# Performance work log

Measured on AMD Instinct MI355X. Metric: run time of the kernel, lower is better.

The kernel has to match this reference:

```python
import jax, jax.numpy as jnp
import numpy as np

EPS = 1e-12
SAMPLE_SIZES = (100, 50)  # hardcoded in the torch module


def setup_inputs() -> dict:
    key = jax.random.key(0)
    k1, k2, k3, k4 = jax.random.split(key, 4)
    N, E, C_IN, C_HID, C_OUT = 50000, 1600000, 256, 64, 128
    x = jax.random.normal(k1, (N, C_IN), dtype=jnp.float32)
    edge_index = jax.random.randint(k2, (2, E), 0, N, dtype=jnp.int64)
    W1 = jax.random.normal(k3, (C_IN, C_HID), dtype=jnp.float32) / np.sqrt(C_IN)
    b1 = jnp.zeros((C_HID,), dtype=jnp.float32)
    W2 = jax.random.normal(k4, (C_HID, C_OUT), dtype=jnp.float32) / np.sqrt(C_HID)
    b2 = jnp.zeros((C_OUT,), dtype=jnp.float32)
    return {"x": x, "edge_index": edge_index, "W1": W1, "b1": b1, "W2": W2, "b2": b2}


def _sample_mask(edge_index, num_samples, key):
    """Keep at most num_samples random out-edges per source node (fixed-shape mask)."""
    src = edge_index[0]
    E = src.shape[0]
    pri = jax.random.uniform(key, (E,))
    order = jnp.lexsort((pri, src))            # group by src, random order within group
    src_sorted = src[order]
    first = jnp.searchsorted(src_sorted, src_sorted, side="left")
    rank = jnp.arange(E) - first               # rank within each src group
    keep_sorted = rank < num_samples
    mask = jnp.zeros((E,), dtype=jnp.float32).at[order].set(keep_sorted.astype(jnp.float32))
    return mask


def _gcn_conv(x, edge_index, edge_weight, W, b, num_nodes):
    """PyG GCNConv: self-loops + symmetric deg^-1/2 normalization, aggregate at dst."""
    h = x @ W                                   # [N, out]
    src, dst = edge_index[0], edge_index[1]
    loop = jnp.arange(num_nodes, dtype=src.dtype)
    src_f = jnp.concatenate([src, loop])
    dst_f = jnp.concatenate([dst, loop])
    w_f = jnp.concatenate([edge_weight, jnp.ones((num_nodes,), dtype=edge_weight.dtype)])
    deg = jax.ops.segment_sum(w_f, dst_f, num_segments=num_nodes)
    dinv = jnp.where(deg > 0, jax.lax.rsqrt(jnp.maximum(deg, EPS)), 0.0)
    norm = w_f * dinv[src_f] * dinv[dst_f]      # [E+N]
    msgs = h[src_f] * norm[:, None]             # gather + scale (memory bound)
    out = jax.ops.segment_sum(msgs, dst_f, num_segments=num_nodes)
    return out + b


def reference(x, edge_index, W1, b1, W2, b2):
    num_nodes = x.shape[0]
    skey = jax.random.key(42)
    sk1, sk2 = jax.random.split(skey)
    m1 = _sample_mask(edge_index, SAMPLE_SIZES[0], sk1)
    m2 = _sample_mask(edge_index, SAMPLE_SIZES[1], sk2)
    h = _gcn_conv(x, edge_index, m1, W1, b1, num_nodes)
    h = jax.nn.relu(h)
    h = h / jnp.maximum(jnp.linalg.norm(h, axis=-1, keepdims=True), EPS)  # F.normalize(p=2)
    out = _gcn_conv(h, edge_index, m2, W2, b2, num_nodes)
    return out
```

## Files before the change

### kernel.cpp

```cpp
#include <hip/hip_runtime.h>

typedef unsigned int u32;
typedef unsigned short u16;
typedef unsigned long long u64;
typedef __attribute__((ext_vector_type(8))) short bh8;
typedef __attribute__((ext_vector_type(4))) float f4;

#define HMAX 1024
#define MAXD 128
#define SB_CAP 24576
#define DB_CAP 6144
#define SBCHUNK 2048
#define SPLIT 8
#define G1S 136
#define DROP_CAP 32768

__device__ inline f4 mfma16(bh8 a, bh8 b, f4 c) {
  return __builtin_amdgcn_mfma_f32_16x16x32_bf16(a, b, c, 0, 0, 0);
}

__host__ __device__ inline void tf2x32(u32 k0, u32 k1, u32 x0, u32 x1, u32& o0, u32& o1) {
  u32 ks2 = k0 ^ k1 ^ 0x1BD11BDAu;
#define ROTL32(x,d) (((x)<<(d))|((x)>>(32-(d))))
#define TFR(r) { x0 += x1; x1 = ROTL32(x1,(r)); x1 ^= x0; }
  x0 += k0; x1 += k1;
  TFR(13) TFR(15) TFR(26) TFR(6)
  x0 += k1; x1 += ks2 + 1u;
  TFR(17) TFR(29) TFR(16) TFR(24)
  x0 += ks2; x1 += k0 + 2u;
  TFR(13) TFR(15) TFR(26) TFR(6)
  x0 += k0; x1 += k1 + 3u;
  TFR(17) TFR(29) TFR(16) TFR(24)
  x0 += k1; x1 += ks2 + 4u;
  TFR(13) TFR(15) TFR(26) TFR(6)
  x0 += ks2; x1 += k0 + 5u;
  o0 = x0; o1 = x1;
#undef TFR
#undef ROTL32
}

__device__ inline u16 f2bf(float f) {
  u32 u = __float_as_uint(f);
  return (u16)((u + 0x7FFFu + ((u >> 16) & 1u)) >> 16);
}
__device__ inline float bflo(u32 u) { return __uint_as_float(u << 16); }
__device__ inline float bfhi(u32 u) { return __uint_as_float(u & 0xFFFF0000u); }

struct BinS { u32 lsrc[128]; u32 lbase[128]; u32 ldst[512]; u32 dbase[512]; };
struct GemS { u16 xs[64 * G1S]; u16 ws[64 * G1S]; };

__global__ __launch_bounds__(256) void k_mega1(const int* __restrict__ ei, int E,
                                               const float* __restrict__ x, int N,
                                               const float* __restrict__ W1, const float* __restrict__ W2,
                                               int* __restrict__ srcCnt, u32* __restrict__ srcRec,
                                               int* __restrict__ dstCnt, u64* __restrict__ dstRec,
                                               u16* __restrict__ h1b, u16* __restrict__ W2t, int nBin) {
  __shared__ __align__(16) char smem[sizeof(GemS)];
  int t = threadIdx.x;
  int bid = blockIdx.x;

  if (bid < nBin) {
    BinS& S = *(BinS*)smem;
    if (t < 128) S.lsrc[t] = 0;
    for (int v = t; v < 512; v += 256) S.ldst[v] = 0;
    __syncthreads();
    int lo = bid * SBCHUNK;
    int hi = min(lo + SBCHUNK, E);
    int e0 = lo + 8 * t;
    int nv = min(8, hi - e0); if (nv < 0) nv = 0;
    int sv[8], dv[8];
    if (nv == 8 && ((E & 3) == 0)) {
      int4 a0 = *((const int4*)(ei + e0));
      int4 a1 = *((const int4*)(ei + e0 + 4));
      int4 b0 = *((const int4*)(ei + E + e0));
      int4 b1 = *((const int4*)(ei + E + e0 + 4));
      sv[0]=a0.x; sv[1]=a0.y; sv[2]=a0.z; sv[3]=a0.w; sv[4]=a1.x; sv[5]=a1.y; sv[6]=a1.z; sv[7]=a1.w;
      dv[0]=b0.x; dv[1]=b0.y; dv[2]=b0.z; dv[3]=b0.w; dv[4]=b1.x; dv[5]=b1.y; dv[6]=b1.z; dv[7]=b1.w;
    } else {
      for (int j = 0; j < nv; ++j) { sv[j] = ei[e0 + j]; dv[j] = ei[E + e0 + j]; }
    }
    for (int j = 0; j < nv; ++j) {
      atomicAdd(&S.lsrc[sv[j] >> 9], 1u);
      atomicAdd(&S.ldst[dv[j] >> 7], 1u);
    }
    __syncthreads();
    if (t < 128) {
      u32 c = S.lsrc[t];
      if (c) S.lbase[t] = (u32)atomicAdd(&srcCnt[t], (int)c);
      S.lsrc[t] = 0;
    }
    for (int v = t; v < 512; v += 256) {
      u32 cd = S.ldst[v];
      if (cd) S.dbase[v] = (u32)atomicAdd(&dstCnt[v], (int)cd);
      S.ldst[v] = 0;
    }
    __syncthreads();
    for (int j = 0; j < nv; ++j) {
      int s = sv[j], d = dv[j];
      u32 i = (u32)(e0 + j);
      int bs = s >> 9;
      u32 slot = S.lbase[bs] + atomicAdd(&S.lsrc[bs], 1u);
      if (slot < SB_CAP) srcRec[(size_t)bs * SB_CAP + slot] = ((u32)(s & 511) << 21) | i;
      int bd = d >> 7;
      u32 slot2 = S.dbase[bd] + atomicAdd(&S.ldst[bd], 1u);
      if (slot2 < DB_CAP)
        dstRec[(size_t)bd * DB_CAP + slot2] = ((u64)(d & 127) << 37) | ((u64)(u32)s << 21) | i;
    }
  } else if (bid < 2 * nBin) {
    GemS& G = *(GemS*)smem;
    int wv = t >> 6, lane = t & 63;
    int qd = lane >> 4, md = lane & 15;
    int m0 = (bid - nBin) * 64;
    if (m0 >= N) return;
    f4 acc[4] = {};
    for (int ks = 0; ks < 256; ks += 128) {
      __syncthreads();
#pragma unroll
      for (int i = 0; i < 8; ++i) {
        int f = t + 256 * i;
        int r = f >> 5, c4 = f & 31;
        int grow = m0 + r; if (grow >= N) grow = N - 1;
        float4 v = ((const float4*)x)[(size_t)grow * 64 + (ks >> 2) + c4];
        u32 p0 = (u32)f2bf(v.x) | ((u32)f2bf(v.y) << 16);
        u32 p1 = (u32)f2bf(v.z) | ((u32)f2bf(v.w) << 16);
        *((uint2*)(G.xs + r * G1S + c4 * 4)) = make_uint2(p0, p1);
      }
#pragma unroll
      for (int i = 0; i < 8; ++i) {
        int f = t + 256 * i;
        int k = f >> 4, c4 = f & 15;
        float4 v = ((const float4*)W1)[(ks + k) * 16 + c4];
        int n0 = c4 * 4;
        G.ws[(n0 + 0) * G1S + k] = f2bf(v.x);
        G.ws[(n0 + 1) * G1S + k] = f2bf(v.y);
        G.ws[(n0 + 2) * G1S + k] = f2bf(v.z);
        G.ws[(n0 + 3) * G1S + k] = f2bf(v.w);
      }
      __syncthreads();
#pragma unroll
      for (int kk = 0; kk < 128; kk += 32) {
        bh8 af = *((const bh8*)(G.xs + (16 * wv + md) * G1S + kk + qd * 8));
#pragma unroll
        for (int nt = 0; nt < 4; ++nt) {
          bh8 bf = *((const bh8*)(G.ws + (nt * 16 + md) * G1S + kk + qd * 8));
          acc[nt] = mfma16(af, bf, acc[nt]);
        }
      }
    }
#pragma unroll
    for (int nt = 0; nt < 4; ++nt)
#pragma unroll
      for (int r = 0; r < 4; ++r) {
        int row = m0 + 16 * wv + qd * 4 + r;
        if (row < N) h1b[(size_t)row * 64 + nt * 16 + md] = f2bf(acc[nt][r]);
      }
  } else {
    for (int e = t; e < 64 * 128; e += 256) {
      int n = e & 127, k = e >> 7;
      W2t[n * 64 + k] = f2bf(W2[k * 128 + n]);
    }
  }
}

__global__ __launch_bounds__(256) void k_shist(const int* __restrict__ srcCnt, const u32* __restrict__ srcRec,
                                               int* __restrict__ outdegB) {
  int bk = blockIdx.x >> 3;
  int part = blockIdx.x & (SPLIT - 1);
  int total = min(srcCnt[bk], SB_CAP);
  int lo = total * part / SPLIT;
  int hi = total * (part + 1) / SPLIT;
  __shared__ u32 cnt[512];
  int t = threadIdx.x;
  cnt[t] = 0; cnt[t + 256] = 0;
  __syncthreads();
  const u32* R = srcRec + (size_t)bk * SB_CAP;
  for (int i = lo + t; i < hi; i += 256) atomicAdd(&cnt[R[i] >> 21], 1u);
  __syncthreads();
  int base = bk * 512;
  for (int v = t; v < 512; v += 256) {
    u32 c = cnt[v];
    if (c) atomicAdd(&outdegB[base + v], (int)c);
  }
}

__global__ __launch_bounds__(256) void k_hdetect(const int* __restrict__ outdegB, u32* __restrict__ idAB,
                                                 int* __restrict__ hcA, int* __restrict__ hcB,
                                                 const int* __restrict__ dstCnt, int* __restrict__ bucketBase,
                                                 int* __restrict__ dptr, int nbD, int N) {
  if (blockIdx.x == 0 && threadIdx.x == 0) {
    int s = 0;
    for (int i = 0; i < nbD; ++i) { bucketBase[i] = s; s += min(dstCnt[i], DB_CAP); }
    bucketBase[nbD] = s;
    dptr[N] = s;
  }
  int v = blockIdx.x * 256 + threadIdx.x;
  if (v >= N) return;
  int dg = outdegB[v];
  u32 pk = 0;
  if (dg > 50) {
    int idb = atomicAdd(hcB, 1);
    if (idb < HMAX) pk = (u32)(idb + 1);
    if (dg > 100) {
      int ida = atomicAdd(hcA, 1);
      if (ida < HMAX) pk |= (u32)(ida + 1) << 16;
    }
  }
  idAB[v] = pk;
}

__global__ __launch_bounds__(256) void k_hfill(const int* __restrict__ srcCnt, const u32* __restrict__ srcRec,
                                               const u32* __restrict__ idAB,
                                               int* __restrict__ bcA, u64* __restrict__ bukA,
                                               int* __restrict__ bcB, u64* __restrict__ bukB,
                                               u32 kaA, u32 kbA, u32 kaB, u32 kbB) {
  int bk = blockIdx.x >> 3;
  int part = blockIdx.x & (SPLIT - 1);
  int total = min(srcCnt[bk], SB_CAP);
  int lo = total * part / SPLIT;
  int hi = total * (part + 1) / SPLIT;
  const u32* R = srcRec + (size_t)bk * SB_CAP;
  int base = bk * 512;
  for (int i = lo + threadIdx.x; i < hi; i += 256) {
    u32 r = R[i];
    u32 pk = idAB[base + (int)(r >> 21)];
    if (pk) {
      u32 e = r & 0x1FFFFFu;
      int idb = (int)(pk & 0xFFFFu) - 1;
      if (idb >= 0) {
        u32 w0, w1; tf2x32(kaB, kbB, 0u, e, w0, w1);
        int slot = atomicAdd(&bcB[idb], 1);
        if (slot < MAXD) bukB[(size_t)idb * MAXD + slot] = ((u64)((w0 ^ w1) >> 9) << 32) | e;
      }
      int ida = (int)(pk >> 16) - 1;
      if (ida >= 0) {
        u32 w0, w1; tf2x32(kaA, kbA, 0u, e, w0, w1);
        int slot = atomicAdd(&bcA[ida], 1);
        if (slot < MAXD) bukA[(size_t)ida * MAXD + slot] = ((u64)((w0 ^ w1) >> 9) << 32) | e;
      }
    }
  }
}

__global__ __launch_bounds__(256) void k_rank2(const int* __restrict__ hcA, const int* __restrict__ bcA,
                                               const u64* __restrict__ bukA,
                                               const int* __restrict__ hcB, const int* __restrict__ bcB,
                                               const u64* __restrict__ bukB,
                                               int* __restrict__ dropCnt, u32* __restrict__ dropList) {
  bool isA = blockIdx.x < (HMAX / 4);
  int bx = isA ? blockIdx.x : blockIdx.x - HMAX / 4;
  const int* hcount = isA ? hcA : hcB;
  const int* bcount = isA ? bcA : bcB;
  const u64* bucket = isA ? bukA : bukB;
  int S = isA ? 100 : 50;
  u32 bit = isA ? 1u : 2u;
  int wid = (bx * 256 + (int)threadIdx.x) >> 6;
  int lane = threadIdx.x & 63;
  int hc = hcount[0]; if (hc > HMAX) hc = HMAX;
  if (wid >= hc) return;
  int d = bcount[wid]; if (d > MAXD) d = MAXD;
  const u64* B = bucket + (size_t)wid * MAXD;
  for (int i = lane; i < d; i += 64) {
    u64 ki = B[i];
    int rank = 0;
    for (int j = 0; j < d; ++j) rank += (B[j] < ki) ? 1 : 0;
    if (rank >= S) {
      int idx = atomicAdd(dropCnt, 1);
      if (idx < DROP_CAP) dropList[idx] = ((u32)ki & 0x1FFFFFu) | (bit << 21);
    }
  }
}

__global__ __launch_bounds__(256) void k_phase2(const int* __restrict__ bucketBase,
                                                const int* __restrict__ dstCnt,
                                                const u64* __restrict__ dstRec,
                                                const int* __restrict__ dropCnt,
                                                const u32* __restrict__ dropList,
                                                u32* __restrict__ entries, int* __restrict__ dptr,
                                                float* __restrict__ dinv1, float* __restrict__ dinv2, int N) {
  int b = blockIdx.x;
  int base = bucketBase[b];
  int cnt0 = min(dstCnt[b], DB_CAP);
  const u64* R = dstRec + (size_t)b * DB_CAP;
  __shared__ u32 cnt[128];
  __shared__ u32 htab[4096];
  __shared__ u32 ws2[2];
  int t = threadIdx.x;
  if (t < 128) cnt[t] = 0;
  for (int i = t; i < 4096; i += 256) htab[i] = 0xFFFFFFFFu;
  __syncthreads();
  int dc = min(dropCnt[0], 3072);
  for (int i = t; i < dc; i += 256) {
    u32 pk = dropList[i];
    u32 key = pk & 0x1FFFFFu;
    u32 h = (key * 2654435761u) >> 20;
    while (true) {
      u32 old = atomicCAS(&htab[h], 0xFFFFFFFFu, pk);
      if (old == 0xFFFFFFFFu) break;
      if ((old & 0x1FFFFFu) == key) { atomicOr(&htab[h], pk & 0x00600000u); break; }
      h = (h + 1) & 4095;
    }
  }
  __syncthreads();
  for (int i = t; i < cnt0; i += 256) {
    u64 r = R[i];
    u32 dl = (u32)(r >> 37) & 127u;
    u32 key = (u32)r & 0x1FFFFFu;
    u32 drop = 0;
    u32 h = (key * 2654435761u) >> 20;
    while (true) {
      u32 v = htab[h];
      if (v == 0xFFFFFFFFu) break;
      if ((v & 0x1FFFFFu) == key) { drop = (v >> 21) & 3u; break; }
      h = (h + 1) & 4095;
    }
    u32 add = 1u + ((1u - (drop & 1u)) << 10) + ((1u - ((drop >> 1) & 1u)) << 20);
    atomicAdd(&cnt[dl], add);
  }
  __syncthreads();
  u32 c0 = (t < 128) ? cnt[t] : 0;
  u32 tot = c0 & 1023u;
  int lane = t & 63, w = t >> 6;
  u32 incl = tot;
  for (int off = 1; off < 64; off <<= 1) {
    u32 nbv = (u32)__shfl_up((int)incl, off, 64);
    if (lane >= off) incl += nbv;
  }
  if (lane == 63 && w == 0) ws2[0] = incl;
  __syncthreads();
  u32 excl = incl - tot + ((w == 1) ? ws2[0] : 0u);
  int v0 = b * 128 + t;
  if (t < 128 && v0 < N) {
    dptr[v0] = base + (int)excl;
    dinv1[v0] = 1.0f / sqrtf((float)(((c0 >> 10) & 1023u) + 1u));
    dinv2[v0] = 1.0f / sqrtf((float)(((c0 >> 20) & 1023u) + 1u));
  }
  __syncthreads();
  if (t < 128) cnt[t] = excl;
  __syncthreads();
  for (int i = t; i < cnt0; i += 256) {
    u64 r = R[i];
    u32 dl = (u32)(r >> 37) & 127u;
    u32 key = (u32)r & 0x1FFFFFu;
    u32 drop = 0;
    u32 h = (key * 2654435761u) >> 20;
    while (true) {
      u32 v = htab[h];
      if (v == 0xFFFFFFFFu) break;
      if ((v & 0x1FFFFFu) == key) { drop = (v >> 21) & 3u; break; }
      h = (h + 1) & 4095;
    }
    u32 src = (u32)(r >> 21) & 0xFFFFu;
    u32 slot = atomicAdd(&cnt[dl], 1u);
    entries[base + slot] = src | ((drop & 1u) ? 0u : (1u << 30)) | ((drop & 2u) ? 0u : (1u << 31));
  }
}

__global__ __launch_bounds__(256) void k_conv1n(const int* __restrict__ ptr, const u32* __restrict__ entries,
                                                const float* __restrict__ dinv1, const uint4* __restrict__ h1q,
                                                const float* __restrict__ b1, uint4* __restrict__ hnbq, int N) {
  int wid = (blockIdx.x * 256 + threadIdx.x) >> 6;
  if (wid >= N) return;
  int lane = threadIdx.x & 63;
  int lo8 = lane & 7, grp = lane >> 3;
  int beg = ptr[wid], end = ptr[wid + 1];
  float a0 = 0.f, a1 = 0.f, a2 = 0.f, a3 = 0.f, a4 = 0.f, a5 = 0.f, a6 = 0.f, a7 = 0.f;
  for (int cb = beg; cb < end; cb += 64) {
    int idx = cb + lane;
    float wgt = 0.f; int s = 0;
    if (idx < end) {
      u32 e = entries[idx];
      s = (int)(e & 0xFFFFu);
      if (e & (1u << 30)) wgt = dinv1[s];
    }
    int nq = (min(64, end - cb) + 7) >> 3;
    int j = grp;
    float w = __shfl(wgt, j, 64);
    int sj = __shfl(s, j, 64);
    uint4 uv = h1q[(size_t)sj * 8 + lo8];
    for (int i = 1; i < nq; ++i) {
      int j2 = j + 8;
      float w2 = __shfl(wgt, j2, 64);
      int s2 = __shfl(s, j2, 64);
      uint4 uv2 = h1q[(size_t)s2 * 8 + lo8];
      a0 = fmaf(w, bflo(uv.x), a0); a1 = fmaf(w, bfhi(uv.x), a1);
      a2 = fmaf(w, bflo(uv.y), a2); a3 = fmaf(w, bfhi(uv.y), a3);
      a4 = fmaf(w, bflo(uv.z), a4); a5 = fmaf(w, bfhi(uv.z), a5);
      a6 = fmaf(w, bflo(uv.w), a6); a7 = fmaf(w, bfhi(uv.w), a7);
      w = w2; uv = uv2; j = j2;
    }
    a0 = fmaf(w, bflo(uv.x), a0); a1 = fmaf(w, bfhi(uv.x), a1);
    a2 = fmaf(w, bflo(uv.y), a2); a3 = fmaf(w, bfhi(uv.y), a3);
    a4 = fmaf(w, bflo(uv.z), a4); a5 = fmaf(w, bfhi(uv.z), a5);
    a6 = fmaf(w, bflo(uv.w), a6); a7 = fmaf(w, bfhi(uv.w), a7);
  }
#pragma unroll
  for (int off = 8; off < 64; off <<= 1) {
    a0 += __shfl_xor(a0, off, 64); a1 += __shfl_xor(a1, off, 64);
    a2 += __shfl_xor(a2, off, 64); a3 += __shfl_xor(a3, off, 64);
    a4 += __shfl_xor(a4, off, 64); a5 += __shfl_xor(a5, off, 64);
    a6 += __shfl_xor(a6, off, 64); a7 += __shfl_xor(a7, off, 64);
  }
  float dv = dinv1[wid];
  uint4 uo = h1q[(size_t)wid * 8 + lo8];
  a0 = fmaf(dv, bflo(uo.x), a0); a1 = fmaf(dv, bfhi(uo.x), a1);
  a2 = fmaf(dv, bflo(uo.y), a2); a3 = fmaf(dv, bfhi(uo.y), a3);
  a4 = fmaf(dv, bflo(uo.z), a4); a5 = fmaf(dv, bfhi(uo.z), a5);
  a6 = fmaf(dv, bflo(uo.w), a6); a7 = fmaf(dv, bfhi(uo.w), a7);
  float4 bbA = ((const float4*)b1)[lo8 * 2];
  float4 bbB = ((const float4*)b1)[lo8 * 2 + 1];
  float o0 = fmaxf(fmaf(dv, a0, bbA.x), 0.f);
  float o1 = fmaxf(fmaf(dv, a1, bbA.y), 0.f);
  float o2 = fmaxf(fmaf(dv, a2, bbA.z), 0.f);
  float o3 = fmaxf(fmaf(dv, a3, bbA.w), 0.f);
  float o4 = fmaxf(fmaf(dv, a4, bbB.x), 0.f);
  float o5 = fmaxf(fmaf(dv, a5, bbB.y), 0.f);
  float o6 = fmaxf(fmaf(dv, a6, bbB.z), 0.f);
  float o7 = fmaxf(fmaf(dv, a7, bbB.w), 0.f);
  float ss = fmaf(o0, o0, fmaf(o1, o1, fmaf(o2, o2, o3 * o3)))
           + fmaf(o4, o4, fmaf(o5, o5, fmaf(o6, o6, o7 * o7)));
#pragma unroll
  for (int off = 1; off < 8; off <<= 1) ss += __shfl_xor(ss, off, 8);
  float sc = 1.f / fmaxf(sqrtf(ss), 1e-12f);
  if (lane < 8) {
    uint4 pv;
    pv.x = (u32)f2bf(o0 * sc) | ((u32)f2bf(o1 * sc) << 16);
    pv.y = (u32)f2bf(o2 * sc) | ((u32)f2bf(o3 * sc) << 16);
    pv.z = (u32)f2bf(o4 * sc) | ((u32)f2bf(o5 * sc) << 16);
    pv.w = (u32)f2bf(o6 * sc) | ((u32)f2bf(o7 * sc) << 16);
    hnbq[(size_t)wid * 8 + lo8] = pv;
  }
}

__global__ __launch_bounds__(256) void k_agg2(const int* __restrict__ ptr, const u32* __restrict__ entries,
                                              const float* __restrict__ dinv2, const uint4* __restrict__ hnq,
                                              uint4* __restrict__ agg2q, int N) {
  int wid = (blockIdx.x * 256 + threadIdx.x) >> 6;
  if (wid >= N) return;
  int lane = threadIdx.x & 63;
  int lo8 = lane & 7, grp = lane >> 3;
  int beg = ptr[wid], end = ptr[wid + 1];
  float a0 = 0.f, a1 = 0.f, a2 = 0.f, a3 = 0.f, a4 = 0.f, a5 = 0.f, a6 = 0.f, a7 = 0.f;
  for (int cb = beg; cb < end; cb += 64) {
    int idx = cb + lane;
    float wgt = 0.f; int s = 0;
    if (idx < end) {
      u32 e = entries[idx];
      s = (int)(e & 0xFFFFu);
      if (e & (1u << 31)) wgt = dinv2[s];
    }
    int nq = (min(64, end - cb) + 7) >> 3;
    int j = grp;
    float w = __shfl(wgt, j, 64);
    int sj = __shfl(s, j, 64);
    uint4 uv = hnq[(size_t)sj * 8 + lo8];
    for (int i = 1; i < nq; ++i) {
      int j2 = j + 8;
      float w2 = __shfl(wgt, j2, 64);
      int s2 = __shfl(s, j2, 64);
      uint4 uv2 = hnq[(size_t)s2 * 8 + lo8];
      a0 = fmaf(w, bflo(uv.x), a0); a1 = fmaf(w, bfhi(uv.x), a1);
      a2 = fmaf(w, bflo(uv.y), a2); a3 = fmaf(w, bfhi(uv.y), a3);
      a4 = fmaf(w, bflo(uv.z), a4); a5 = fmaf(w, bfhi(uv.z), a5);
      a6 = fmaf(w, bflo(uv.w), a6); a7 = fmaf(w, bfhi(uv.w), a7);
      w = w2; uv = uv2; j = j2;
    }
    a0 = fmaf(w, bflo(uv.x), a0); a1 = fmaf(w, bfhi(uv.x), a1);
    a2 = fmaf(w, bflo(uv.y), a2); a3 = fmaf(w, bfhi(uv.y), a3);
    a4 = fmaf(w, bflo(uv.z), a4); a5 = fmaf(w, bfhi(uv.z), a5);
    a6 = fmaf(w, bflo(uv.w), a6); a7 = fmaf(w, bfhi(uv.w), a7);
  }
#pragma unroll
  for (int off = 8; off < 64; off <<= 1) {
    a0 += __shfl_xor(a0, off, 64); a1 += __shfl_xor(a1, off, 64);
    a2 += __shfl_xor(a2, off, 64); a3 += __shfl_xor(a3, off, 64);
    a4 += __shfl_xor(a4, off, 64); a5 += __shfl_xor(a5, off, 64);
    a6 += __shfl_xor(a6, off, 64); a7 += __shfl_xor(a7, off, 64);
  }
  float dv = dinv2[wid];
  uint4 uo = hnq[(size_t)wid * 8 + lo8];
  a0 = fmaf(dv, bflo(uo.x), a0); a1 = fmaf(dv, bfhi(uo.x), a1);
  a2 = fmaf(dv, bflo(uo.y), a2); a3 = fmaf(dv, bfhi(uo.y), a3);
  a4 = fmaf(dv, bflo(uo.z), a4); a5 = fmaf(dv, bfhi(uo.z), a5);
  a6 = fmaf(dv, bflo(uo.w), a6); a7 = fmaf(dv, bfhi(uo.w), a7);
  if (lane < 8) {
    uint4 pv;
    pv.x = (u32)f2bf(dv * a0) | ((u32)f2bf(dv * a1) << 16);
    pv.y = (u32)f2bf(dv * a2) | ((u32)f2bf(dv * a3) << 16);
    pv.z = (u32)f2bf(dv * a4) | ((u32)f2bf(dv * a5) << 16);
    pv.w = (u32)f2bf(dv * a6) | ((u32)f2bf(dv * a7) << 16);
    agg2q[(size_t)wid * 8 + lo8] = pv;
  }
}

#define G2S 72
__global__ __launch_bounds__(256) void k_gemm2f(const u16* __restrict__ aggb, const u16* __restrict__ W2t,
                                                const float* __restrict__ b2, float* __restrict__ out, int N) {
  __shared__ u16 hs[64 * G2S];
  __shared__ u16 ws[128 * G2S];
  int t = threadIdx.x;
  int wv = t >> 6, lane = t & 63;
  int qd = lane >> 4, md = lane & 15;
  int m0 = blockIdx.x * 64;
#pragma unroll
  for (int i = 0; i < 2; ++i) {
    int cc = t + 256 * i;
    int r = cc >> 3, kc = (cc & 7) * 8;
    int grow = m0 + r; if (grow >= N) grow = N - 1;
    *((uint4*)(hs + r * G2S + kc)) = *((const uint4*)(aggb + (size_t)grow * 64 + kc));
  }
#pragma unroll
  for (int i = 0; i < 4; ++i) {
    int cc = t + 256 * i;
    int n = cc >> 3, kc = (cc & 7) * 8;
    *((uint4*)(ws + n * G2S + kc)) = *((const uint4*)(W2t + n * 64 + kc));
  }
  __syncthreads();
  f4 acc[8] = {};
#pragma unroll
  for (int kk = 0; kk < 64; kk += 32) {
    bh8 af = *((const bh8*)(hs + (16 * wv + md) * G2S + kk + qd * 8));
#pragma unroll
    for (int nt = 0; nt < 8; ++nt) {
      bh8 bf = *((const bh8*)(ws + (nt * 16 + md) * G2S + kk + qd * 8));
      acc[nt] = mfma16(af, bf, acc[nt]);
    }
  }
#pragma unroll
  for (int nt = 0; nt < 8; ++nt) {
    float bv = b2[nt * 16 + md];
#pragma unroll
    for (int r = 0; r < 4; ++r) {
      int row = m0 + 16 * wv + qd * 4 + r;
      if (row < N) out[(size_t)row * 128 + nt * 16 + md] = acc[nt][r] + bv;
    }
  }
}

extern "C" void kernel_launch(void* const* d_in, const int* in_sizes, int n_in,
                              void* d_out, int out_size, void* d_ws, size_t ws_size,
                              hipStream_t stream) {
  const float* x  = (const float*)d_in[0];
  const int*   ei = (const int*)d_in[1];
  const float* W1 = (const float*)d_in[2];
  const float* b1 = (const float*)d_in[3];
  const float* W2 = (const float*)d_in[4];
  const float* b2 = (const float*)d_in[5];
  const int N = in_sizes[0] / 256;
  const int E = in_sizes[1] / 2;
  const int nbS = (N + 511) >> 9;
  const int nbD = (N + 127) >> 7;

  u32 sk1a, sk1b, sk2a, sk2b;
  tf2x32(0u, 42u, 0u, 0u, sk1a, sk1b);
  tf2x32(0u, 42u, 0u, 1u, sk2a, sk2b);

  char* p = (char*)d_ws;
  auto alloc = [&](size_t bytes) { char* r = p; p += (bytes + 255) & ~(size_t)255; return r; };
  int* dstCnt      = (int*)alloc(512 * 4);
  int* srcCnt      = (int*)alloc(128 * 4);
  int* hcbA        = (int*)alloc((size_t)(1 + HMAX) * 4);
  int* hcbB        = (int*)alloc((size_t)(1 + HMAX) * 4);
  int* outdegB     = (int*)alloc((size_t)nbS * 512 * 4);
  int* dropCnt     = (int*)alloc(256);
  char* zero_end = p;
  u32* dropList = (u32*)alloc((size_t)DROP_CAP * 4);
  u32* idAB     = (u32*)alloc((size_t)nbS * 512 * 4);
  u16* h1b      = (u16*)alloc((size_t)N * 64 * 2);
  u16* hnb      = (u16*)alloc((size_t)N * 64 * 2);
  u16* agg2b    = (u16*)alloc((size_t)N * 64 * 2);
  float* dinv1  = (float*)alloc((size_t)N * 4);
  float* dinv2  = (float*)alloc((size_t)N * 4);
  int* dptr     = (int*)alloc((size_t)(N + 1) * 4);
  int* bucketBase = (int*)alloc(513 * 4);
  u32* entries  = (u32*)alloc((size_t)E * 4);
  u32* srcRec   = (u32*)alloc((size_t)nbS * SB_CAP * 4);
  u64* dstRec   = (u64*)alloc((size_t)nbD * DB_CAP * 8);
  u64* bukA     = (u64*)alloc((size_t)HMAX * MAXD * 8);
  u64* bukB     = (u64*)alloc((size_t)HMAX * MAXD * 8);
  u16* W2t      = (u16*)alloc(64 * 128 * 2);

  int* hcA = hcbA; int* bcA = hcbA + 1;
  int* hcB = hcbB; int* bcB = hcbB + 1;

  hipMemsetAsync(dstCnt, 0x00, (size_t)(zero_end - (char*)dstCnt), stream);

  const int nBin = (E + SBCHUNK - 1) / SBCHUNK;
  const int nGemm = (N + 63) / 64;
  k_mega1<<<nBin + nGemm + 1, 256, 0, stream>>>(ei, E, x, N, W1, W2,
                                                srcCnt, srcRec, dstCnt, dstRec, h1b, W2t, nBin);
  k_shist<<<nbS * SPLIT, 256, 0, stream>>>(srcCnt, srcRec, outdegB);
  k_hdetect<<<(N + 255) / 256, 256, 0, stream>>>(outdegB, idAB, hcA, hcB, dstCnt, bucketBase,
                                                 dptr, nbD, N);
  k_hfill<<<nbS * SPLIT, 256, 0, stream>>>(srcCnt, srcRec, idAB, bcA, bukA, bcB, bukB,
                                           sk1a, sk1b, sk2a, sk2b);
  k_rank2<<<HMAX / 2, 256, 0, stream>>>(hcA, bcA, bukA, hcB, bcB, bukB, dropCnt, dropList);
  k_phase2<<<nbD, 256, 0, stream>>>(bucketBase, dstCnt, dstRec, dropCnt, dropList,
                                    entries, dptr, dinv1, dinv2, N);
  k_conv1n<<<(N * 64 + 255) / 256, 256, 0, stream>>>(dptr, entries, dinv1, (const uint4*)h1b, b1,
                                                     (uint4*)hnb, N);
  k_agg2<<<(N * 64 + 255) / 256, 256, 0, stream>>>(dptr, entries, dinv2, (const uint4*)hnb,
                                                   (uint4*)agg2b, N);
  k_gemm2f<<<(N + 63) / 64, 256, 0, stream>>>(agg2b, W2t, b2, (float*)d_out, N);
}
```

Baseline: 303.8 us.

## Drop source-binning pass; count out-degree with global atomics and scan edges directly

Replaces the source-bucket record scatter and the separate histogram kernel with direct global atomic increments of per-node out-degree inside the binning kernel. The hub-fill kernel now streams the raw source array instead of the binned records. This removes a kernel launch plus the srcRec write and two reads of it, in exchange for 1.6M scattered global atomics and a grid-stride scan over all edges. The first GEMM also switches to a 64-wide K tile with smaller LDS (stride 72), which raises occupancy but adds more sync steps; it also fixes the GEMM block range to use nGemm.

```diff
diff --git a/kernel.cpp b/kernel.cpp
--- a/kernel.cpp
+++ b/kernel.cpp
@@ -8,11 +8,9 @@
 
 #define HMAX 1024
 #define MAXD 128
-#define SB_CAP 24576
 #define DB_CAP 6144
 #define SBCHUNK 2048
-#define SPLIT 8
-#define G1S 136
+#define G1S 72
 #define DROP_CAP 32768
 
 __device__ inline f4 mfma16(bh8 a, bh8 b, f4 c) {
@@ -46,22 +44,22 @@
 __device__ inline float bflo(u32 u) { return __uint_as_float(u << 16); }
 __device__ inline float bfhi(u32 u) { return __uint_as_float(u & 0xFFFF0000u); }
 
-struct BinS { u32 lsrc[128]; u32 lbase[128]; u32 ldst[512]; u32 dbase[512]; };
+struct BinS { u32 ldst[512]; u32 dbase[512]; };
 struct GemS { u16 xs[64 * G1S]; u16 ws[64 * G1S]; };
 
 __global__ __launch_bounds__(256) void k_mega1(const int* __restrict__ ei, int E,
                                                const float* __restrict__ x, int N,
                                                const float* __restrict__ W1, const float* __restrict__ W2,
-                                               int* __restrict__ srcCnt, u32* __restrict__ srcRec,
+                                               int* __restrict__ outdeg,
                                                int* __restrict__ dstCnt, u64* __restrict__ dstRec,
                                                u16* __restrict__ h1b, u16* __restrict__ W2t, int nBin) {
   __shared__ __align__(16) char smem[sizeof(GemS)];
   int t = threadIdx.x;
   int bid = blockIdx.x;
+  int nGemm = (N + 63) >> 6;
 
   if (bid < nBin) {
     BinS& S = *(BinS*)smem;
-    if (t < 128) S.lsrc[t] = 0;
     for (int v = t; v < 512; v += 256) S.ldst[v] = 0;
     __syncthreads();
     int lo = bid * SBCHUNK;
@@ -80,15 +78,10 @@
       for (int j = 0; j < nv; ++j) { sv[j] = ei[e0 + j]; dv[j] = ei[E + e0 + j]; }
     }
     for (int j = 0; j < nv; ++j) {
-      atomicAdd(&S.lsrc[sv[j] >> 9], 1u);
+      atomicAdd(&outdeg[sv[j]], 1);
       atomicAdd(&S.ldst[dv[j] >> 7], 1u);
     }
     __syncthreads();
-    if (t < 128) {
-      u32 c = S.lsrc[t];
-      if (c) S.lbase[t] = (u32)atomicAdd(&srcCnt[t], (int)c);
-      S.lsrc[t] = 0;
-    }
     for (int v = t; v < 512; v += 256) {
       u32 cd = S.ldst[v];
       if (cd) S.dbase[v] = (u32)atomicAdd(&dstCnt[v], (int)cd);
@@ -98,27 +91,24 @@
     for (int j = 0; j < nv; ++j) {
       int s = sv[j], d = dv[j];
       u32 i = (u32)(e0 + j);
-      int bs = s >> 9;
-      u32 slot = S.lbase[bs] + atomicAdd(&S.lsrc[bs], 1u);
-      if (slot < SB_CAP) srcRec[(size_t)bs * SB_CAP + slot] = ((u32)(s & 511) << 21) | i;
       int bd = d >> 7;
       u32 slot2 = S.dbase[bd] + atomicAdd(&S.ldst[bd], 1u);
       if (slot2 < DB_CAP)
         dstRec[(size_t)bd * DB_CAP + slot2] = ((u64)(d & 127) << 37) | ((u64)(u32)s << 21) | i;
     }
-  } else if (bid < 2 * nBin) {
+  } else if (bid < nBin + nGemm) {
     GemS& G = *(GemS*)smem;
     int wv = t >> 6, lane = t & 63;
     int qd = lane >> 4, md = lane & 15;
     int m0 = (bid - nBin) * 64;
     if (m0 >= N) return;
     f4 acc[4] = {};
-    for (int ks = 0; ks < 256; ks += 128) {
+    for (int ks = 0; ks < 256; ks += 64) {
       __syncthreads();
 #pragma unroll
-      for (int i = 0; i < 8; ++i) {
+      for (int i = 0; i < 4; ++i) {
         int f = t + 256 * i;
-        int r = f >> 5, c4 = f & 31;
+        int r = f >> 4, c4 = f & 15;
         int grow = m0 + r; if (grow >= N) grow = N - 1;
         float4 v = ((const float4*)x)[(size_t)grow * 64 + (ks >> 2) + c4];
         u32 p0 = (u32)f2bf(v.x) | ((u32)f2bf(v.y) << 16);
@@ -126,7 +116,7 @@
         *((uint2*)(G.xs + r * G1S + c4 * 4)) = make_uint2(p0, p1);
       }
 #pragma unroll
-      for (int i = 0; i < 8; ++i) {
+      for (int i = 0; i < 4; ++i) {
         int f = t + 256 * i;
         int k = f >> 4, c4 = f & 15;
         float4 v = ((const float4*)W1)[(ks + k) * 16 + c4];
@@ -138,7 +128,7 @@
       }
       __syncthreads();
 #pragma unroll
-      for (int kk = 0; kk < 128; kk += 32) {
+      for (int kk = 0; kk < 64; kk += 32) {
         bh8 af = *((const bh8*)(G.xs + (16 * wv + md) * G1S + kk + qd * 8));
 #pragma unroll
         for (int nt = 0; nt < 4; ++nt) {
@@ -162,28 +152,7 @@
   }
 }
 
-__global__ __launch_bounds__(256) void k_shist(const int* __restrict__ srcCnt, const u32* __restrict__ srcRec,
-                                               int* __restrict__ outdegB) {
-  int bk = blockIdx.x >> 3;
-  int part = blockIdx.x & (SPLIT - 1);
-  int total = min(srcCnt[bk], SB_CAP);
-  int lo = total * part / SPLIT;
-  int hi = total * (part + 1) / SPLIT;
-  __shared__ u32 cnt[512];
-  int t = threadIdx.x;
-  cnt[t] = 0; cnt[t + 256] = 0;
-  __syncthreads();
-  const u32* R = srcRec + (size_t)bk * SB_CAP;
-  for (int i = lo + t; i < hi; i += 256) atomicAdd(&cnt[R[i] >> 21], 1u);
-  __syncthreads();
-  int base = bk * 512;
-  for (int v = t; v < 512; v += 256) {
-    u32 c = cnt[v];
-    if (c) atomicAdd(&outdegB[base + v], (int)c);
-  }
-}
-
-__global__ __launch_bounds__(256) void k_hdetect(const int* __restrict__ outdegB, u32* __restrict__ idAB,
+__global__ __launch_bounds__(256) void k_hdetect(const int* __restrict__ outdeg, u32* __restrict__ idAB,
                                                  int* __restrict__ hcA, int* __restrict__ hcB,
                                                  const int* __restrict__ dstCnt, int* __restrict__ bucketBase,
                                                  int* __restrict__ dptr, int nbD, int N) {
@@ -195,7 +164,7 @@
   }
   int v = blockIdx.x * 256 + threadIdx.x;
   if (v >= N) return;
-  int dg = outdegB[v];
+  int dg = outdeg[v];
   u32 pk = 0;
   if (dg > 50) {
     int idb = atomicAdd(hcB, 1);
@@ -208,34 +177,27 @@
   idAB[v] = pk;
 }
 
-__global__ __launch_bounds__(256) void k_hfill(const int* __restrict__ srcCnt, const u32* __restrict__ srcRec,
+__global__ __launch_bounds__(256) void k_hfill(const int* __restrict__ ei, int E,
                                                const u32* __restrict__ idAB,
                                                int* __restrict__ bcA, u64* __restrict__ bukA,
                                                int* __restrict__ bcB, u64* __restrict__ bukB,
                                                u32 kaA, u32 kbA, u32 kaB, u32 kbB) {
-  int bk = blockIdx.x >> 3;
-  int part = blockIdx.x & (SPLIT - 1);
-  int total = min(srcCnt[bk], SB_CAP);
-  int lo = total * part / SPLIT;
-  int hi = total * (part + 1) / SPLIT;
-  const u32* R = srcRec + (size_t)bk * SB_CAP;
-  int base = bk * 512;
-  for (int i = lo + threadIdx.x; i < hi; i += 256) {
-    u32 r = R[i];
-    u32 pk = idAB[base + (int)(r >> 21)];
+  for (int e = blockIdx.x * 256 + (int)threadIdx.x; e < E; e += (int)gridDim.x * 256) {
+    int s = ei[e];
+    u32 pk = idAB[s];
     if (pk) {
-      u32 e = r & 0x1FFFFFu;
+      u32 eu = (u32)e;
       int idb = (int)(pk & 0xFFFFu) - 1;
       if (idb >= 0) {
-        u32 w0, w1; tf2x32(kaB, kbB, 0u, e, w0, w1);
+        u32 w0, w1; tf2x32(kaB, kbB, 0u, eu, w0, w1);
         int slot = atomicAdd(&bcB[idb], 1);
-        if (slot < MAXD) bukB[(size_t)idb * MAXD + slot] = ((u64)((w0 ^ w1) >> 9) << 32) | e;
+        if (slot < MAXD) bukB[(size_t)idb * MAXD + slot] = ((u64)((w0 ^ w1) >> 9) << 32) | eu;
       }
       int ida = (int)(pk >> 16) - 1;
       if (ida >= 0) {
-        u32 w0, w1; tf2x32(kaA, kbA, 0u, e, w0, w1);
+        u32 w0, w1; tf2x32(kaA, kbA, 0u, eu, w0, w1);
         int slot = atomicAdd(&bcA[ida], 1);
-        if (slot < MAXD) bukA[(size_t)ida * MAXD + slot] = ((u64)((w0 ^ w1) >> 9) << 32) | e;
+        if (slot < MAXD) bukA[(size_t)ida * MAXD + slot] = ((u64)((w0 ^ w1) >> 9) << 32) | eu;
       }
     }
   }
@@ -547,7 +509,6 @@
   const float* b2 = (const float*)d_in[5];
   const int N = in_sizes[0] / 256;
   const int E = in_sizes[1] / 2;
-  const int nbS = (N + 511) >> 9;
   const int nbD = (N + 127) >> 7;
 
   u32 sk1a, sk1b, sk2a, sk2b;
@@ -557,14 +518,13 @@
   char* p = (char*)d_ws;
   auto alloc = [&](size_t bytes) { char* r = p; p += (bytes + 255) & ~(size_t)255; return r; };
   int* dstCnt      = (int*)alloc(512 * 4);
-  int* srcCnt      = (int*)alloc(128 * 4);
   int* hcbA        = (int*)alloc((size_t)(1 + HMAX) * 4);
   int* hcbB        = (int*)alloc((size_t)(1 + HMAX) * 4);
-  int* outdegB     = (int*)alloc((size_t)nbS * 512 * 4);
   int* dropCnt     = (int*)alloc(256);
+  int* outdeg      = (int*)alloc((size_t)N * 4);
   char* zero_end = p;
   u32* dropList = (u32*)alloc((size_t)DROP_CAP * 4);
-  u32* idAB     = (u32*)alloc((size_t)nbS * 512 * 4);
+  u32* idAB     = (u32*)alloc((size_t)N * 4);
   u16* h1b      = (u16*)alloc((size_t)N * 64 * 2);
   u16* hnb      = (u16*)alloc((size_t)N * 64 * 2);
   u16* agg2b    = (u16*)alloc((size_t)N * 64 * 2);
@@ -573,7 +533,6 @@
   int* dptr     = (int*)alloc((size_t)(N + 1) * 4);
   int* bucketBase = (int*)alloc(513 * 4);
   u32* entries  = (u32*)alloc((size_t)E * 4);
-  u32* srcRec   = (u32*)alloc((size_t)nbS * SB_CAP * 4);
   u64* dstRec   = (u64*)alloc((size_t)nbD * DB_CAP * 8);
   u64* bukA     = (u64*)alloc((size_t)HMAX * MAXD * 8);
   u64* bukB     = (u64*)alloc((size_t)HMAX * MAXD * 8);
@@ -587,12 +546,11 @@
   const int nBin = (E + SBCHUNK - 1) / SBCHUNK;
   const int nGemm = (N + 63) / 64;
   k_mega1<<<nBin + nGemm + 1, 256, 0, stream>>>(ei, E, x, N, W1, W2,
-                                                srcCnt, srcRec, dstCnt, dstRec, h1b, W2t, nBin);
-  k_shist<<<nbS * SPLIT, 256, 0, stream>>>(srcCnt, srcRec, outdegB);
-  k_hdetect<<<(N + 255) / 256, 256, 0, stream>>>(outdegB, idAB, hcA, hcB, dstCnt, bucketBase,
+                                                outdeg, dstCnt, dstRec, h1b, W2t, nBin);
+  k_hdetect<<<(N + 255) / 256, 256, 0, stream>>>(outdeg, idAB, hcA, hcB, dstCnt, bucketBase,
                                                  dptr, nbD, N);
-  k_hfill<<<nbS * SPLIT, 256, 0, stream>>>(srcCnt, srcRec, idAB, bcA, bukA, bcB, bukB,
-                                           sk1a, sk1b, sk2a, sk2b);
+  k_hfill<<<2048, 256, 0, stream>>>(ei, E, idAB, bcA, bukA, bcB, bukB,
+                                    sk1a, sk1b, sk2a, sk2b);
   k_rank2<<<HMAX / 2, 256, 0, stream>>>(hcA, bcA, bukA, hcB, bcB, bukB, dropCnt, dropList);
   k_phase2<<<nbD, 256, 0, stream>>>(bucketBase, dstCnt, dstRec, dropCnt, dropList,
                                     entries, dptr, dinv1, dinv2, N);
```

Result: slower. 342.2 us (+12.6%).
